# Performance work log

Hardware: AMD Instinct MI355X
Metric: run time of the kernel (lower is better)

## Reference

```python
import jax, jax.numpy as jnp
import numpy as np

B, S, H, L, NH, FF, V = 16, 512, 768, 12, 12, 3072, 30522
D = H // NH


def _ln(x, g, b, eps=1e-12):
    mu = jnp.mean(x, -1, keepdims=True)
    var = jnp.var(x, -1, keepdims=True)
    return (x - mu) / jnp.sqrt(var + eps) * g + b


def setup_inputs() -> dict:
    key = jax.random.key(0)
    ks = jax.random.split(key, 24)
    w = lambda k, shape: jax.random.normal(k, shape, jnp.float32) * 0.02
    inp = {}
    inp['input_ids'] = jax.random.randint(ks[0], (B, S), 0, V)
    inp['token_type_ids'] = jax.random.randint(ks[1], (B, S), 0, 2)
    inp['attention_mask'] = jnp.ones((B, S), jnp.float32)
    inp['importance_scores'] = jax.random.uniform(ks[2], (B, S), jnp.float32)
    inp['noise'] = jax.random.normal(ks[3], (B, S, H), jnp.float32)  # std = self.std = 1.0
    # embedding tables + embedding LayerNorm
    inp['word_emb'] = w(ks[4], (V, H))
    inp['pos_emb'] = w(ks[5], (512, H))
    inp['type_emb'] = w(ks[6], (2, H))
    inp['emb_ln_g'] = jnp.ones((H,), jnp.float32)
    inp['emb_ln_b'] = jnp.zeros((H,), jnp.float32)
    # stacked per-layer encoder params [L, ...]
    inp['Wq'] = w(ks[7], (L, H, H)); inp['bq'] = jnp.zeros((L, H), jnp.float32)
    inp['Wk'] = w(ks[8], (L, H, H)); inp['bk'] = jnp.zeros((L, H), jnp.float32)
    inp['Wv'] = w(ks[9], (L, H, H)); inp['bv'] = jnp.zeros((L, H), jnp.float32)
    inp['Wo'] = w(ks[10], (L, H, H)); inp['bo'] = jnp.zeros((L, H), jnp.float32)
    inp['ln1_g'] = jnp.ones((L, H), jnp.float32); inp['ln1_b'] = jnp.zeros((L, H), jnp.float32)
    inp['Wi'] = w(ks[11], (L, H, FF)); inp['bi'] = jnp.zeros((L, FF), jnp.float32)
    inp['Wd'] = w(ks[12], (L, FF, H)); inp['bd'] = jnp.zeros((L, H), jnp.float32)
    inp['ln2_g'] = jnp.ones((L, H), jnp.float32); inp['ln2_b'] = jnp.zeros((L, H), jnp.float32)
    # pooler
    inp['pool_w'] = w(ks[13], (H, H)); inp['pool_b'] = jnp.zeros((H,), jnp.float32)
    return inp


def reference(input_ids, token_type_ids, attention_mask, importance_scores, noise,
              word_emb, pos_emb, type_emb, emb_ln_g, emb_ln_b,
              Wq, bq, Wk, bk, Wv, bv, Wo, bo, ln1_g, ln1_b,
              Wi, bi, Wd, bd, ln2_g, ln2_b, pool_w, pool_b):
    seq = input_ids.shape[1]
    # bert embeddings (dropout is a no-op at eval)
    emb = word_emb[input_ids] + pos_emb[:seq][None, :, :] + type_emb[token_type_ids]
    emb = _ln(emb, emb_ln_g, emb_ln_b)
    # vectorized equivalent of the per-token GaussianNoise loop (soft_suff):
    # sigma = 1 - importance; noise scaled by sigma * detach(embedding); only where importance != 0
    imp = jax.lax.stop_gradient(importance_scores)  # .clone().detach()
    sigma = (1.0 - imp)[..., None]
    noisy = emb + noise * sigma * jax.lax.stop_gradient(emb)
    emb = jnp.where((imp != 0.0)[..., None], noisy, emb)
    ext_mask = (1.0 - attention_mask)[:, None, None, :] * -10000.0  # [B,1,1,S]
    x = emb * 1.0  # ig = 1

    def block(x, p):
        wq, bq_, wk, bk_, wv, bv_, wo, bo_, g1, b1, wi, bi_, wd, bd_, g2, b2 = p
        q = (x @ wq + bq_).reshape(B, S, NH, D)
        k = (x @ wk + bk_).reshape(B, S, NH, D)
        v = (x @ wv + bv_).reshape(B, S, NH, D)
        scores = jnp.einsum('bqhd,bkhd->bhqk', q, k) / np.sqrt(D).astype(np.float32) + ext_mask
        probs = jax.nn.softmax(scores, axis=-1)
        ctx = jnp.einsum('bhqk,bkhd->bqhd', probs, v).reshape(B, S, H)
        x = _ln(x + ctx @ wo + bo_, g1, b1)
        h = jax.nn.gelu(x @ wi + bi_, approximate=False) @ wd + bd_
        x = _ln(x + h, g2, b2)
        return x, None

    x, _ = jax.lax.scan(block, x, (Wq, bq, Wk, bk, Wv, bv, Wo, bo, ln1_g, ln1_b,
                                   Wi, bi, Wd, bd, ln2_g, ln2_b))
    pooled = jnp.tanh(x[:, 0] @ pool_w + pool_b)
    return x, pooled
```

## Files before the change

### kernel.cpp

```cpp
#include <hip/hip_runtime.h>

typedef unsigned short u16;
typedef unsigned int u32;
typedef __attribute__((ext_vector_type(8))) short bf16x8;
typedef __attribute__((ext_vector_type(4))) float f32x4;

__device__ __forceinline__ u16 f2bf(float v) {
  u32 x = __builtin_bit_cast(u32, v);
  x += 0x7FFFu + ((x >> 16) & 1u);
  return (u16)(x >> 16);
}

__device__ __forceinline__ float block_sum(float v, float* buf) {
#pragma unroll
  for (int m = 32; m >= 1; m >>= 1) v += __shfl_xor(v, m);
  int w = threadIdx.x >> 6;
  if ((threadIdx.x & 63) == 0) buf[w] = v;
  __syncthreads();
  v = buf[0] + buf[1] + buf[2] + buf[3];
  __syncthreads();
  return v;
}

__global__ __launch_bounds__(256) void keybias_kernel(const float* __restrict__ mask,
                                                      float* __restrict__ kb, int n) {
  int i = blockIdx.x * 256 + threadIdx.x;
  if (i < n) kb[i] = (1.0f - mask[i]) * -10000.0f;
}

__global__ __launch_bounds__(256)
void embed_ln_kernel(const int* __restrict__ ids, const int* __restrict__ tts,
                     const float* __restrict__ imp, const float* __restrict__ noise,
                     const float* __restrict__ wemb, const float* __restrict__ pemb,
                     const float* __restrict__ temb, const float* __restrict__ g,
                     const float* __restrict__ bb, float* __restrict__ x,
                     u16* __restrict__ xb) {
  __shared__ float buf[4];
  long t = blockIdx.x;
  int s = (int)(t & 511);
  int tid = threadIdx.x;
  long id = ids[t], tt = tts[t];
  float e[3];
#pragma unroll
  for (int i = 0; i < 3; ++i) {
    int d = tid + i * 256;
    e[i] = wemb[id * 768 + d] + pemb[(long)s * 768 + d] + temb[tt * 768 + d];
  }
  float mu = block_sum(e[0] + e[1] + e[2], buf) * (1.0f / 768.0f);
  float vs = 0.f;
#pragma unroll
  for (int i = 0; i < 3; ++i) { float dd = e[i] - mu; vs += dd * dd; }
  float inv = rsqrtf(block_sum(vs, buf) * (1.0f / 768.0f) + 1e-12f);
  float ip = imp[t];
  float sig = 1.0f - ip;
  bool app = (ip != 0.0f);
#pragma unroll
  for (int i = 0; i < 3; ++i) {
    int d = tid + i * 256;
    float y = (e[i] - mu) * inv * g[d] + bb[d];
    if (app) y = y * (1.0f + noise[t * 768 + d] * sig);
    x[t * 768 + d] = y;
    xb[t * 768 + d] = f2bf(y);
  }
}

__global__ __launch_bounds__(256)
void ln_res_kernel(const float* __restrict__ xin, const float* __restrict__ yin,
                   const float* __restrict__ g, const float* __restrict__ bb,
                   float* __restrict__ xout, u16* __restrict__ xbout) {
  __shared__ float buf[4];
  long t = blockIdx.x;
  int tid = threadIdx.x;
  float e[3];
#pragma unroll
  for (int i = 0; i < 3; ++i) {
    int d = tid + i * 256;
    e[i] = xin[t * 768 + d] + yin[t * 768 + d];
  }
  float mu = block_sum(e[0] + e[1] + e[2], buf) * (1.0f / 768.0f);
  float vs = 0.f;
#pragma unroll
  for (int i = 0; i < 3; ++i) { float dd = e[i] - mu; vs += dd * dd; }
  float inv = rsqrtf(block_sum(vs, buf) * (1.0f / 768.0f) + 1e-12f);
#pragma unroll
  for (int i = 0; i < 3; ++i) {
    int d = tid + i * 256;
    float v = (e[i] - mu) * inv * g[d] + bb[d];
    xout[t * 768 + d] = v;
    xbout[t * 768 + d] = f2bf(v);
  }
}

__global__ __launch_bounds__(256)
void convert_w_kernel(const float* __restrict__ wq, const float* __restrict__ wk,
                      const float* __restrict__ wv, const float* __restrict__ wo,
                      const float* __restrict__ wi, const float* __restrict__ wd,
                      u16* __restrict__ wqkvob, u16* __restrict__ wib,
                      u16* __restrict__ wdb) {
  __shared__ float tile[32][33];
  int t = blockIdx.x;
  const float* in;
  u16* outp;
  int Kd, Nd, kt, nt;
  if (t < 2304) {
    int m = t / 576, lt = t % 576;
    in = (m == 0) ? wq : (m == 1) ? wk : (m == 2) ? wv : wo;
    outp = wqkvob + (long)m * 589824;
    Kd = 768; Nd = 768; kt = lt / 24; nt = lt % 24;
  } else if (t < 4608) {
    int lt = t - 2304;
    in = wi; outp = wib; Kd = 768; Nd = 3072; kt = lt / 96; nt = lt % 96;
  } else {
    int lt = t - 4608;
    in = wd; outp = wdb; Kd = 3072; Nd = 768; kt = lt / 24; nt = lt % 24;
  }
  int tx = threadIdx.x, ty = threadIdx.y;
#pragma unroll
  for (int i = 0; i < 4; ++i)
    tile[ty + i * 8][tx] = in[(long)(kt * 32 + ty + i * 8) * Nd + nt * 32 + tx];
  __syncthreads();
#pragma unroll
  for (int i = 0; i < 4; ++i)
    outp[(long)(nt * 32 + ty + i * 8) * Kd + kt * 32 + tx] = f2bf(tile[tx][ty + i * 8]);
}

__global__ __launch_bounds__(256)
void transpose_v_kernel(const u16* __restrict__ vb, u16* __restrict__ vtb) {
  __shared__ u16 tile[32][33];
  int s0 = blockIdx.x * 32, d0 = blockIdx.y * 32;
  int b = blockIdx.z / 12, h = blockIdx.z % 12;
  int tx = threadIdx.x, ty = threadIdx.y;
#pragma unroll
  for (int i = 0; i < 4; ++i)
    tile[ty + i * 8][tx] = vb[(long)(b * 512 + s0 + ty + i * 8) * 768 + h * 64 + d0 + tx];
  __syncthreads();
#pragma unroll
  for (int i = 0; i < 4; ++i)
    vtb[(long)((b * 12 + h) * 64 + d0 + ty + i * 8) * 512 + s0 + tx] = tile[tx][ty + i * 8];
}

template <int EPI, bool OBF16>
__global__ __launch_bounds__(256)
void gemm_kernel(const u16* __restrict__ A, const u16* __restrict__ Bmat, long strideB,
                 const float* __restrict__ bias0, const float* __restrict__ bias1,
                 const float* __restrict__ bias2, void* __restrict__ Out, long strideOut,
                 int M, int N, int K) {
  __shared__ __align__(16) u16 As[128][40];
  __shared__ __align__(16) u16 Bs[128][40];
  int z = blockIdx.z;
  const u16* B = Bmat + (long)z * strideB;
  const float* bias = (z == 0) ? bias0 : ((z == 1) ? bias1 : bias2);
  int m0 = blockIdx.x * 128, n0 = blockIdx.y * 128;
  int tid = threadIdx.x;
  int w = tid >> 6, lane = tid & 63;
  int wr = (w >> 1) * 64, wc = (w & 1) * 64;
  int quad = lane >> 4, l16 = lane & 15;
  f32x4 acc[4][4] = {};
  for (int kk = 0; kk < K; kk += 32) {
#pragma unroll
    for (int i = 0; i < 2; ++i) {
      int c = tid + i * 256;
      int row = c >> 2, kc = c & 3;
      *(uint4*)&As[row][kc * 8] = *(const uint4*)&A[(long)(m0 + row) * K + kk + kc * 8];
      *(uint4*)&Bs[row][kc * 8] = *(const uint4*)&B[(long)(n0 + row) * K + kk + kc * 8];
    }
    __syncthreads();
    bf16x8 af[4], bfv[4];
#pragma unroll
    for (int i = 0; i < 4; ++i) af[i] = *(const bf16x8*)&As[wr + i * 16 + l16][quad * 8];
#pragma unroll
    for (int j = 0; j < 4; ++j) bfv[j] = *(const bf16x8*)&Bs[wc + j * 16 + l16][quad * 8];
#pragma unroll
    for (int i = 0; i < 4; ++i)
#pragma unroll
      for (int j = 0; j < 4; ++j)
        acc[i][j] = __builtin_amdgcn_mfma_f32_16x16x32_bf16(af[i], bfv[j], acc[i][j], 0, 0, 0);
    __syncthreads();
  }
#pragma unroll
  for (int i = 0; i < 4; ++i) {
#pragma unroll
    for (int j = 0; j < 4; ++j) {
      int n = n0 + wc + j * 16 + l16;
      float bv = bias[n];
#pragma unroll
      for (int r = 0; r < 4; ++r) {
        int m = m0 + wr + i * 16 + quad * 4 + r;
        float v = acc[i][j][r] + bv;
        if (EPI == 2) v = v * 0.5f * (1.0f + erff(v * 0.70710678118654752f));
        long idx = (long)z * strideOut + (long)m * N + n;
        if (OBF16) ((u16*)Out)[idx] = f2bf(v);
        else ((float*)Out)[idx] = v;
      }
    }
  }
}

__global__ __launch_bounds__(256)
void attn_kernel(const u16* __restrict__ qb, const u16* __restrict__ kb,
                 const u16* __restrict__ vtb, const float* __restrict__ keybias,
                 u16* __restrict__ ctxb) {
  __shared__ __align__(16) u16 Ks[64][72];
  __shared__ __align__(16) u16 Vts[64][72];
  __shared__ __align__(16) u16 Ps[4][16][72];
  int qt = blockIdx.x, h = blockIdx.y, b = blockIdx.z;
  int tid = threadIdx.x, w = tid >> 6, lane = tid & 63;
  int quad = lane >> 4, l16 = lane & 15;
  long qrow = (long)(b * 512 + qt * 64 + w * 16 + l16);
  bf16x8 qf0 = *(const bf16x8*)&qb[qrow * 768 + h * 64 + quad * 8];
  bf16x8 qf1 = *(const bf16x8*)&qb[qrow * 768 + h * 64 + 32 + quad * 8];
  f32x4 accO[4] = {};
  float mi[4], li[4];
#pragma unroll
  for (int r = 0; r < 4; ++r) { mi[r] = -1e30f; li[r] = 0.f; }
  for (int kt = 0; kt < 8; ++kt) {
    __syncthreads();
#pragma unroll
    for (int i = 0; i < 2; ++i) {
      int c = tid + i * 256;
      int row = c >> 3, dc = c & 7;
      *(uint4*)&Ks[row][dc * 8] =
          *(const uint4*)&kb[(long)(b * 512 + kt * 64 + row) * 768 + h * 64 + dc * 8];
      *(uint4*)&Vts[row][dc * 8] =
          *(const uint4*)&vtb[(long)((b * 12 + h) * 64 + row) * 512 + kt * 64 + dc * 8];
    }
    __syncthreads();
    f32x4 s[4] = {};
#pragma unroll
    for (int j = 0; j < 4; ++j) {
      bf16x8 kf0 = *(const bf16x8*)&Ks[j * 16 + l16][quad * 8];
      s[j] = __builtin_amdgcn_mfma_f32_16x16x32_bf16(qf0, kf0, s[j], 0, 0, 0);
      bf16x8 kf1 = *(const bf16x8*)&Ks[j * 16 + l16][32 + quad * 8];
      s[j] = __builtin_amdgcn_mfma_f32_16x16x32_bf16(qf1, kf1, s[j], 0, 0, 0);
    }
#pragma unroll
    for (int j = 0; j < 4; ++j) {
      float kbv = keybias[b * 512 + kt * 64 + j * 16 + l16];
#pragma unroll
      for (int r = 0; r < 4; ++r) s[j][r] = s[j][r] * 0.125f + kbv;
    }
#pragma unroll
    for (int r = 0; r < 4; ++r) {
      float mx = fmaxf(fmaxf(s[0][r], s[1][r]), fmaxf(s[2][r], s[3][r]));
      mx = fmaxf(mx, __shfl_xor(mx, 1));
      mx = fmaxf(mx, __shfl_xor(mx, 2));
      mx = fmaxf(mx, __shfl_xor(mx, 4));
      mx = fmaxf(mx, __shfl_xor(mx, 8));
      float mn = fmaxf(mi[r], mx);
      float alpha = __expf(mi[r] - mn);
      float ps = 0.f;
#pragma unroll
      for (int j = 0; j < 4; ++j) { s[j][r] = __expf(s[j][r] - mn); ps += s[j][r]; }
      ps += __shfl_xor(ps, 1);
      ps += __shfl_xor(ps, 2);
      ps += __shfl_xor(ps, 4);
      ps += __shfl_xor(ps, 8);
      li[r] = li[r] * alpha + ps;
      mi[r] = mn;
#pragma unroll
      for (int j = 0; j < 4; ++j) accO[j][r] *= alpha;
    }
#pragma unroll
    for (int j = 0; j < 4; ++j)
#pragma unroll
      for (int r = 0; r < 4; ++r)
        Ps[w][quad * 4 + r][j * 16 + l16] = f2bf(s[j][r]);
    __syncthreads();
#pragma unroll
    for (int kk = 0; kk < 2; ++kk) {
      bf16x8 pf = *(const bf16x8*)&Ps[w][l16][kk * 32 + quad * 8];
#pragma unroll
      for (int j = 0; j < 4; ++j) {
        bf16x8 vf = *(const bf16x8*)&Vts[j * 16 + l16][kk * 32 + quad * 8];
        accO[j] = __builtin_amdgcn_mfma_f32_16x16x32_bf16(pf, vf, accO[j], 0, 0, 0);
      }
    }
  }
#pragma unroll
  for (int j = 0; j < 4; ++j)
#pragma unroll
    for (int r = 0; r < 4; ++r) {
      float v = accO[j][r] / li[r];
      long row = (long)(b * 512 + qt * 64 + w * 16 + quad * 4 + r);
      ctxb[row * 768 + h * 64 + j * 16 + l16] = f2bf(v);
    }
}

__global__ __launch_bounds__(256)
void pooler_kernel(const float* __restrict__ xfin, const float* __restrict__ pw,
                   const float* __restrict__ pb, float* __restrict__ outp) {
  __shared__ float xr[768];
  int o = blockIdx.x * 256 + threadIdx.x;
  int b = blockIdx.y;
  for (int i = threadIdx.x; i < 768; i += 256) xr[i] = xfin[(long)b * 512 * 768 + i];
  __syncthreads();
  float acc = pb[o];
  for (int k = 0; k < 768; ++k) acc += xr[k] * pw[(long)k * 768 + o];
  outp[(long)b * 768 + o] = tanhf(acc);
}

extern "C" void kernel_launch(void* const* d_in, const int* in_sizes, int n_in,
                              void* d_out, int out_size, void* d_ws, size_t ws_size,
                              hipStream_t stream) {
  const int* ids = (const int*)d_in[0];
  const int* tts = (const int*)d_in[1];
  const float* amask = (const float*)d_in[2];
  const float* imp = (const float*)d_in[3];
  const float* noise = (const float*)d_in[4];
  const float* wemb = (const float*)d_in[5];
  const float* pemb = (const float*)d_in[6];
  const float* temb = (const float*)d_in[7];
  const float* elng = (const float*)d_in[8];
  const float* elnb = (const float*)d_in[9];
  const float* Wq = (const float*)d_in[10];
  const float* bq = (const float*)d_in[11];
  const float* Wk = (const float*)d_in[12];
  const float* bk = (const float*)d_in[13];
  const float* Wv = (const float*)d_in[14];
  const float* bv = (const float*)d_in[15];
  const float* Wo = (const float*)d_in[16];
  const float* bo = (const float*)d_in[17];
  const float* ln1g = (const float*)d_in[18];
  const float* ln1b = (const float*)d_in[19];
  const float* Wi = (const float*)d_in[20];
  const float* bi = (const float*)d_in[21];
  const float* Wd = (const float*)d_in[22];
  const float* bd = (const float*)d_in[23];
  const float* ln2g = (const float*)d_in[24];
  const float* ln2b = (const float*)d_in[25];
  const float* poolw = (const float*)d_in[26];
  const float* poolb = (const float*)d_in[27];
  float* out = (float*)d_out;

  const long T = 8192;
  char* p = (char*)d_ws;
  auto carve = [&](size_t bytes) -> void* {
    void* r = (void*)p;
    p += (bytes + 255) & ~(size_t)255;
    return r;
  };
  float* x = (float*)carve(T * 768 * 4);
  float* y = (float*)carve(T * 768 * 4);
  u16* xb = (u16*)carve(T * 768 * 2);
  u16* qkvb = (u16*)carve(3 * T * 768 * 2);
  u16* vtb = (u16*)carve(T * 768 * 2);
  u16* ctxb = (u16*)carve(T * 768 * 2);
  u16* hb = (u16*)carve(T * 3072 * 2);
  u16* wqkvob = (u16*)carve(4L * 589824 * 2);
  u16* wib = (u16*)carve(2359296L * 2);
  u16* wdb = (u16*)carve(2359296L * 2);
  float* kbias = (float*)carve(T * 4);
  if ((size_t)(p - (char*)d_ws) > ws_size) return;

  keybias_kernel<<<(int)(T / 256), 256, 0, stream>>>(amask, kbias, (int)T);
  embed_ln_kernel<<<(int)T, 256, 0, stream>>>(ids, tts, imp, noise, wemb, pemb, temb,
                                              elng, elnb, x, xb);

  for (int l = 0; l < 12; ++l) {
    convert_w_kernel<<<6912, dim3(32, 8), 0, stream>>>(
        Wq + (long)l * 589824, Wk + (long)l * 589824, Wv + (long)l * 589824,
        Wo + (long)l * 589824, Wi + (long)l * 2359296, Wd + (long)l * 2359296,
        wqkvob, wib, wdb);
    gemm_kernel<1, true><<<dim3(64, 6, 3), 256, 0, stream>>>(
        xb, wqkvob, 589824L, bq + (long)l * 768, bk + (long)l * 768, bv + (long)l * 768,
        (void*)qkvb, T * 768, 8192, 768, 768);
    transpose_v_kernel<<<dim3(16, 2, 192), dim3(32, 8), 0, stream>>>(qkvb + 2 * T * 768, vtb);
    attn_kernel<<<dim3(8, 12, 16), 256, 0, stream>>>(qkvb, qkvb + T * 768, vtb, kbias, ctxb);
    gemm_kernel<1, false><<<dim3(64, 6, 1), 256, 0, stream>>>(
        ctxb, wqkvob + 3L * 589824, 0L, bo + (long)l * 768, bo + (long)l * 768,
        bo + (long)l * 768, (void*)y, 0L, 8192, 768, 768);
    ln_res_kernel<<<(int)T, 256, 0, stream>>>(x, y, ln1g + (long)l * 768,
                                              ln1b + (long)l * 768, x, xb);
    gemm_kernel<2, true><<<dim3(64, 24, 1), 256, 0, stream>>>(
        xb, wib, 0L, bi + (long)l * 3072, bi + (long)l * 3072, bi + (long)l * 3072,
        (void*)hb, 0L, 8192, 3072, 768);
    gemm_kernel<1, false><<<dim3(64, 6, 1), 256, 0, stream>>>(
        hb, wdb, 0L, bd + (long)l * 768, bd + (long)l * 768, bd + (long)l * 768,
        (void*)y, 0L, 8192, 768, 3072);
    float* xo = (l == 11) ? out : x;
    ln_res_kernel<<<(int)T, 256, 0, stream>>>(x, y, ln2g + (long)l * 768,
                                              ln2b + (long)l * 768, xo, xb);
  }
  pooler_kernel<<<dim3(3, 16), 256, 0, stream>>>(out, poolw, poolb, out + T * 768);
}
```

Baseline: 4.103 ms.

## Use direct global-to-LDS GEMM loads, split-K output GEMMs, wave-per-row LayerNorm

The GEMM now loads tiles with global_load_lds straight into an unpadded, XOR-swizzled LDS layout instead of staging through registers. The two N=768 GEMMs (attention output and FFN down) use split-K=2 to double the grid, writing partial sums into a second buffer that aliases the qkv scratch. The residual LayerNorm sums both partials, so no separate reduction pass is needed. LayerNorm and embedding kernels now process one token per wave with float4 accesses and no block barriers, and weight conversion writes packed 16-byte bf16 stores. Risks include the aliasing of y1 onto qkvb and getting the swizzle mapping right.

```diff
diff --git a/kernel.cpp b/kernel.cpp
--- a/kernel.cpp
+++ b/kernel.cpp
@@ -4,6 +4,8 @@
 typedef unsigned int u32;
 typedef __attribute__((ext_vector_type(8))) short bf16x8;
 typedef __attribute__((ext_vector_type(4))) float f32x4;
+typedef __attribute__((ext_vector_type(4))) unsigned short u16x4;
+typedef __attribute__((ext_vector_type(8))) unsigned short u16x8;
 
 __device__ __forceinline__ u16 f2bf(float v) {
   u32 x = __builtin_bit_cast(u32, v);
@@ -11,15 +13,16 @@
   return (u16)(x >> 16);
 }
 
-__device__ __forceinline__ float block_sum(float v, float* buf) {
+__device__ __forceinline__ float wave_sum(float v) {
 #pragma unroll
   for (int m = 32; m >= 1; m >>= 1) v += __shfl_xor(v, m);
-  int w = threadIdx.x >> 6;
-  if ((threadIdx.x & 63) == 0) buf[w] = v;
-  __syncthreads();
-  v = buf[0] + buf[1] + buf[2] + buf[3];
-  __syncthreads();
   return v;
+}
+
+__device__ __forceinline__ void gload_lds16(const u16* g, u16* l) {
+  __builtin_amdgcn_global_load_lds(
+      (const __attribute__((address_space(1))) unsigned int*)g,
+      (__attribute__((address_space(3))) unsigned int*)l, 16, 0, 0);
 }
 
 __global__ __launch_bounds__(256) void keybias_kernel(const float* __restrict__ mask,
@@ -35,59 +38,80 @@
                      const float* __restrict__ temb, const float* __restrict__ g,
                      const float* __restrict__ bb, float* __restrict__ x,
                      u16* __restrict__ xb) {
-  __shared__ float buf[4];
-  long t = blockIdx.x;
+  long t = (long)blockIdx.x * 4 + (threadIdx.x >> 6);
+  int lane = threadIdx.x & 63;
   int s = (int)(t & 511);
-  int tid = threadIdx.x;
   long id = ids[t], tt = tts[t];
-  float e[3];
+  f32x4 e[3];
 #pragma unroll
   for (int i = 0; i < 3; ++i) {
-    int d = tid + i * 256;
-    e[i] = wemb[id * 768 + d] + pemb[(long)s * 768 + d] + temb[tt * 768 + d];
-  }
-  float mu = block_sum(e[0] + e[1] + e[2], buf) * (1.0f / 768.0f);
+    int c4 = i * 64 + lane;
+    e[i] = *(const f32x4*)&wemb[(id * 192 + c4) * 4] + *(const f32x4*)&pemb[((long)s * 192 + c4) * 4]
+         + *(const f32x4*)&temb[(tt * 192 + c4) * 4];
+  }
+  float sm = 0.f;
+#pragma unroll
+  for (int i = 0; i < 3; ++i) sm += e[i][0] + e[i][1] + e[i][2] + e[i][3];
+  float mu = wave_sum(sm) * (1.0f / 768.0f);
   float vs = 0.f;
 #pragma unroll
-  for (int i = 0; i < 3; ++i) { float dd = e[i] - mu; vs += dd * dd; }
-  float inv = rsqrtf(block_sum(vs, buf) * (1.0f / 768.0f) + 1e-12f);
+  for (int i = 0; i < 3; ++i)
+#pragma unroll
+    for (int c = 0; c < 4; ++c) { float d = e[i][c] - mu; vs += d * d; }
+  float inv = rsqrtf(wave_sum(vs) * (1.0f / 768.0f) + 1e-12f);
   float ip = imp[t];
   float sig = 1.0f - ip;
   bool app = (ip != 0.0f);
 #pragma unroll
   for (int i = 0; i < 3; ++i) {
-    int d = tid + i * 256;
-    float y = (e[i] - mu) * inv * g[d] + bb[d];
-    if (app) y = y * (1.0f + noise[t * 768 + d] * sig);
-    x[t * 768 + d] = y;
-    xb[t * 768 + d] = f2bf(y);
-  }
-}
-
-__global__ __launch_bounds__(256)
-void ln_res_kernel(const float* __restrict__ xin, const float* __restrict__ yin,
-                   const float* __restrict__ g, const float* __restrict__ bb,
-                   float* __restrict__ xout, u16* __restrict__ xbout) {
-  __shared__ float buf[4];
-  long t = blockIdx.x;
-  int tid = threadIdx.x;
-  float e[3];
+    int c4 = i * 64 + lane;
+    f32x4 gv = *(const f32x4*)&g[c4 * 4], bv = *(const f32x4*)&bb[c4 * 4];
+    f32x4 o = (e[i] - mu) * inv * gv + bv;
+    if (app) {
+      f32x4 nz = *(const f32x4*)&noise[(t * 192 + c4) * 4];
+      o = o * (1.0f + nz * sig);
+    }
+    *(f32x4*)&x[(t * 192 + c4) * 4] = o;
+    u16x4 pk;
+#pragma unroll
+    for (int c = 0; c < 4; ++c) pk[c] = f2bf(o[c]);
+    *(u16x4*)&xb[(t * 192 + c4) * 4] = pk;
+  }
+}
+
+__global__ __launch_bounds__(256)
+void ln_res_kernel(const float* __restrict__ xin, const float* __restrict__ y0,
+                   const float* __restrict__ y1, const float* __restrict__ g,
+                   const float* __restrict__ bb, float* __restrict__ xout,
+                   u16* __restrict__ xbout) {
+  long t = (long)blockIdx.x * 4 + (threadIdx.x >> 6);
+  int lane = threadIdx.x & 63;
+  f32x4 e[3];
 #pragma unroll
   for (int i = 0; i < 3; ++i) {
-    int d = tid + i * 256;
-    e[i] = xin[t * 768 + d] + yin[t * 768 + d];
-  }
-  float mu = block_sum(e[0] + e[1] + e[2], buf) * (1.0f / 768.0f);
+    long o4 = (t * 192 + i * 64 + lane) * 4;
+    e[i] = *(const f32x4*)&xin[o4] + *(const f32x4*)&y0[o4] + *(const f32x4*)&y1[o4];
+  }
+  float sm = 0.f;
+#pragma unroll
+  for (int i = 0; i < 3; ++i) sm += e[i][0] + e[i][1] + e[i][2] + e[i][3];
+  float mu = wave_sum(sm) * (1.0f / 768.0f);
   float vs = 0.f;
 #pragma unroll
-  for (int i = 0; i < 3; ++i) { float dd = e[i] - mu; vs += dd * dd; }
-  float inv = rsqrtf(block_sum(vs, buf) * (1.0f / 768.0f) + 1e-12f);
+  for (int i = 0; i < 3; ++i)
+#pragma unroll
+    for (int c = 0; c < 4; ++c) { float d = e[i][c] - mu; vs += d * d; }
+  float inv = rsqrtf(wave_sum(vs) * (1.0f / 768.0f) + 1e-12f);
 #pragma unroll
   for (int i = 0; i < 3; ++i) {
-    int d = tid + i * 256;
-    float v = (e[i] - mu) * inv * g[d] + bb[d];
-    xout[t * 768 + d] = v;
-    xbout[t * 768 + d] = f2bf(v);
+    int c4 = i * 64 + lane;
+    f32x4 gv = *(const f32x4*)&g[c4 * 4], bv = *(const f32x4*)&bb[c4 * 4];
+    f32x4 o = (e[i] - mu) * inv * gv + bv;
+    *(f32x4*)&xout[(t * 192 + c4) * 4] = o;
+    u16x4 pk;
+#pragma unroll
+    for (int c = 0; c < 4; ++c) pk[c] = f2bf(o[c]);
+    *(u16x4*)&xbout[(t * 192 + c4) * 4] = pk;
   }
 }
 
@@ -119,9 +143,14 @@
   for (int i = 0; i < 4; ++i)
     tile[ty + i * 8][tx] = in[(long)(kt * 32 + ty + i * 8) * Nd + nt * 32 + tx];
   __syncthreads();
-#pragma unroll
-  for (int i = 0; i < 4; ++i)
-    outp[(long)(nt * 32 + ty + i * 8) * Kd + kt * 32 + tx] = f2bf(tile[tx][ty + i * 8]);
+  int t2 = ty * 32 + tx;
+  if (t2 < 128) {
+    int n = t2 >> 2, kcq = t2 & 3;
+    u16x8 pk;
+#pragma unroll
+    for (int j = 0; j < 8; ++j) pk[j] = f2bf(tile[kcq * 8 + j][n]);
+    *(u16x8*)&outp[(long)(nt * 32 + n) * Kd + kt * 32 + kcq * 8] = pk;
+  }
 }
 
 __global__ __launch_bounds__(256)
@@ -139,37 +168,45 @@
     vtb[(long)((b * 12 + h) * 64 + d0 + ty + i * 8) * 512 + s0 + tx] = tile[tx][ty + i * 8];
 }
 
-template <int EPI, bool OBF16>
-__global__ __launch_bounds__(256)
-void gemm_kernel(const u16* __restrict__ A, const u16* __restrict__ Bmat, long strideB,
+template <int EPI, bool OBF16, bool SPLITK>
+__global__ __launch_bounds__(256)
+void gemm_kernel(const u16* __restrict__ A, const u16* __restrict__ Bmat,
+                 long lda, long ldb, long zoffB,
                  const float* __restrict__ bias0, const float* __restrict__ bias1,
-                 const float* __restrict__ bias2, void* __restrict__ Out, long strideOut,
+                 const float* __restrict__ bias2, void* __restrict__ Out, long zoffOut,
                  int M, int N, int K) {
-  __shared__ __align__(16) u16 As[128][40];
-  __shared__ __align__(16) u16 Bs[128][40];
+  __shared__ __align__(16) u16 As[128 * 32];
+  __shared__ __align__(16) u16 Bs[128 * 32];
   int z = blockIdx.z;
-  const u16* B = Bmat + (long)z * strideB;
-  const float* bias = (z == 0) ? bias0 : ((z == 1) ? bias1 : bias2);
+  long kOff = SPLITK ? (long)z * K : 0;
+  const u16* Bz = Bmat + (SPLITK ? 0L : (long)z * zoffB);
+  const float* bias = SPLITK ? bias0 : ((z == 0) ? bias0 : (z == 1) ? bias1 : bias2);
+  bool addBias = (!SPLITK) || (z == 0);
   int m0 = blockIdx.x * 128, n0 = blockIdx.y * 128;
-  int tid = threadIdx.x;
-  int w = tid >> 6, lane = tid & 63;
+  int tid = threadIdx.x, w = tid >> 6, lane = tid & 63;
+  int quad = lane >> 4, l16 = lane & 15;
+  int srow = 32 * w + (lane >> 2);
+  int kc = (lane & 3) ^ ((lane >> 3) & 3);
+  const u16* aG = A + (long)(m0 + srow) * lda + kOff + kc * 8;
+  const u16* bG = Bz + (long)(n0 + srow) * ldb + kOff + kc * 8;
+  u16* aL0 = &As[(32 * w) * 32];
+  u16* aL1 = &As[(32 * w + 16) * 32];
+  u16* bL0 = &Bs[(32 * w) * 32];
+  u16* bL1 = &Bs[(32 * w + 16) * 32];
+  int slot = (quad ^ ((l16 >> 1) & 3)) * 8;
   int wr = (w >> 1) * 64, wc = (w & 1) * 64;
-  int quad = lane >> 4, l16 = lane & 15;
   f32x4 acc[4][4] = {};
   for (int kk = 0; kk < K; kk += 32) {
-#pragma unroll
-    for (int i = 0; i < 2; ++i) {
-      int c = tid + i * 256;
-      int row = c >> 2, kc = c & 3;
-      *(uint4*)&As[row][kc * 8] = *(const uint4*)&A[(long)(m0 + row) * K + kk + kc * 8];
-      *(uint4*)&Bs[row][kc * 8] = *(const uint4*)&B[(long)(n0 + row) * K + kk + kc * 8];
-    }
+    gload_lds16(aG + kk, aL0);
+    gload_lds16(aG + 16 * lda + kk, aL1);
+    gload_lds16(bG + kk, bL0);
+    gload_lds16(bG + 16 * ldb + kk, bL1);
     __syncthreads();
     bf16x8 af[4], bfv[4];
 #pragma unroll
-    for (int i = 0; i < 4; ++i) af[i] = *(const bf16x8*)&As[wr + i * 16 + l16][quad * 8];
-#pragma unroll
-    for (int j = 0; j < 4; ++j) bfv[j] = *(const bf16x8*)&Bs[wc + j * 16 + l16][quad * 8];
+    for (int i = 0; i < 4; ++i) af[i] = *(const bf16x8*)&As[(wr + i * 16 + l16) * 32 + slot];
+#pragma unroll
+    for (int j = 0; j < 4; ++j) bfv[j] = *(const bf16x8*)&Bs[(wc + j * 16 + l16) * 32 + slot];
 #pragma unroll
     for (int i = 0; i < 4; ++i)
 #pragma unroll
@@ -182,15 +219,15 @@
 #pragma unroll
     for (int j = 0; j < 4; ++j) {
       int n = n0 + wc + j * 16 + l16;
-      float bv = bias[n];
+      float bv = addBias ? bias[n] : 0.0f;
 #pragma unroll
       for (int r = 0; r < 4; ++r) {
         int m = m0 + wr + i * 16 + quad * 4 + r;
         float v = acc[i][j][r] + bv;
         if (EPI == 2) v = v * 0.5f * (1.0f + erff(v * 0.70710678118654752f));
-        long idx = (long)z * strideOut + (long)m * N + n;
-        if (OBF16) ((u16*)Out)[idx] = f2bf(v);
-        else ((float*)Out)[idx] = v;
+        long idx = (long)m * N + n;
+        if (OBF16) ((u16*)Out)[(long)z * zoffOut + idx] = f2bf(v);
+        else ((float*)Out)[(long)z * zoffOut + idx] = v;
       }
     }
   }
@@ -352,34 +389,37 @@
   float* kbias = (float*)carve(T * 4);
   if ((size_t)(p - (char*)d_ws) > ws_size) return;
 
-  keybias_kernel<<<(int)(T / 256), 256, 0, stream>>>(amask, kbias, (int)T);
-  embed_ln_kernel<<<(int)T, 256, 0, stream>>>(ids, tts, imp, noise, wemb, pemb, temb,
-                                              elng, elnb, x, xb);
+  float* y1 = (float*)qkvb;
+  long zoffO = (long)(y1 - y);
+
+  keybias_kernel<<<32, 256, 0, stream>>>(amask, kbias, (int)T);
+  embed_ln_kernel<<<(int)(T / 4), 256, 0, stream>>>(ids, tts, imp, noise, wemb, pemb,
+                                                    temb, elng, elnb, x, xb);
 
   for (int l = 0; l < 12; ++l) {
     convert_w_kernel<<<6912, dim3(32, 8), 0, stream>>>(
         Wq + (long)l * 589824, Wk + (long)l * 589824, Wv + (long)l * 589824,
         Wo + (long)l * 589824, Wi + (long)l * 2359296, Wd + (long)l * 2359296,
         wqkvob, wib, wdb);
-    gemm_kernel<1, true><<<dim3(64, 6, 3), 256, 0, stream>>>(
-        xb, wqkvob, 589824L, bq + (long)l * 768, bk + (long)l * 768, bv + (long)l * 768,
-        (void*)qkvb, T * 768, 8192, 768, 768);
+    gemm_kernel<1, true, false><<<dim3(64, 6, 3), 256, 0, stream>>>(
+        xb, wqkvob, 768, 768, 589824L, bq + (long)l * 768, bk + (long)l * 768,
+        bv + (long)l * 768, (void*)qkvb, T * 768, 8192, 768, 768);
     transpose_v_kernel<<<dim3(16, 2, 192), dim3(32, 8), 0, stream>>>(qkvb + 2 * T * 768, vtb);
     attn_kernel<<<dim3(8, 12, 16), 256, 0, stream>>>(qkvb, qkvb + T * 768, vtb, kbias, ctxb);
-    gemm_kernel<1, false><<<dim3(64, 6, 1), 256, 0, stream>>>(
-        ctxb, wqkvob + 3L * 589824, 0L, bo + (long)l * 768, bo + (long)l * 768,
-        bo + (long)l * 768, (void*)y, 0L, 8192, 768, 768);
-    ln_res_kernel<<<(int)T, 256, 0, stream>>>(x, y, ln1g + (long)l * 768,
-                                              ln1b + (long)l * 768, x, xb);
-    gemm_kernel<2, true><<<dim3(64, 24, 1), 256, 0, stream>>>(
-        xb, wib, 0L, bi + (long)l * 3072, bi + (long)l * 3072, bi + (long)l * 3072,
-        (void*)hb, 0L, 8192, 3072, 768);
-    gemm_kernel<1, false><<<dim3(64, 6, 1), 256, 0, stream>>>(
-        hb, wdb, 0L, bd + (long)l * 768, bd + (long)l * 768, bd + (long)l * 768,
-        (void*)y, 0L, 8192, 768, 3072);
+    gemm_kernel<1, false, true><<<dim3(64, 6, 2), 256, 0, stream>>>(
+        ctxb, wqkvob + 3L * 589824, 768, 768, 0L, bo + (long)l * 768, bo + (long)l * 768,
+        bo + (long)l * 768, (void*)y, zoffO, 8192, 768, 384);
+    ln_res_kernel<<<(int)(T / 4), 256, 0, stream>>>(x, y, y1, ln1g + (long)l * 768,
+                                                    ln1b + (long)l * 768, x, xb);
+    gemm_kernel<2, true, false><<<dim3(64, 24, 1), 256, 0, stream>>>(
+        xb, wib, 768, 768, 0L, bi + (long)l * 3072, bi + (long)l * 3072,
+        bi + (long)l * 3072, (void*)hb, 0L, 8192, 3072, 768);
+    gemm_kernel<1, false, true><<<dim3(64, 6, 2), 256, 0, stream>>>(
+        hb, wdb, 3072, 3072, 0L, bd + (long)l * 768, bd + (long)l * 768,
+        bd + (long)l * 768, (void*)y, zoffO, 8192, 768, 1536);
     float* xo = (l == 11) ? out : x;
-    ln_res_kernel<<<(int)T, 256, 0, stream>>>(x, y, ln2g + (long)l * 768,
-                                              ln2b + (long)l * 768, xo, xb);
+    ln_res_kernel<<<(int)(T / 4), 256, 0, stream>>>(x, y, y1, ln2g + (long)l * 768,
+                                                    ln2b + (long)l * 768, xo, xb);
   }
   pooler_kernel<<<dim3(3, 16), 256, 0, stream>>>(out, poolw, poolb, out + T * 768);
 }
```

Result: faster. 3.811 ms (-7.1%).
